# Performance work log

Hardware: AMD Instinct MI355X
Metric: run time of the kernel (lower is better)

The kernel has to match this reference:

```python
import jax, jax.numpy as jnp
from jax import lax
import numpy as np

NUM_HEADS = 8
PATCH = 16
EPS_SUM = 1e-6


def resize_nearest(x, H, W):
    # torch F.interpolate(mode='nearest'): src = floor(dst * in / out)
    ih, iw = x.shape[-2], x.shape[-1]
    ri = (jnp.arange(H) * ih) // H
    ci = (jnp.arange(W) * iw) // W
    return x[:, :, ri][:, :, :, ci]


def single_scale(x, delta, wq, bq, ws, bs):
    # x: [1+K, C, H, W]; delta: [K, 1, H0, W0]
    q, s = x[:1], x[1:]
    K, C, H, W = s.shape
    d = C // NUM_HEADS
    P = PATCH
    Hp, Wp = H // P, W // P
    S = P * P
    delta = resize_nearest(delta, H, W)  # [K,1,H,W]

    qf = jnp.transpose(q, (0, 2, 3, 1))[0] @ wq.T + bq            # [H,W,C]
    qh = qf.reshape(H, W, NUM_HEADS, d).transpose(2, 0, 1, 3)     # [h,H,W,d]
    sf = jnp.transpose(s, (0, 2, 3, 1)) @ ws.T + bs               # [K,H,W,C]
    sh = sf.reshape(K, H, W, NUM_HEADS, d).transpose(0, 3, 1, 2, 4)  # [K,h,H,W,d]

    fg = delta.reshape(K, P, Hp, P, Wp).transpose(0, 1, 3, 2, 4).reshape(K, S, Hp * Wp)
    bg = 1.0 - fg
    fg_sum = jnp.maximum(fg.sum(-1), EPS_SUM)  # [K,S]
    bg_sum = jnp.maximum(bg.sum(-1), EPS_SUM)

    sp = sh.reshape(K, NUM_HEADS, P, Hp, P, Wp, d).transpose(0, 1, 2, 4, 3, 5, 6)
    sp = sp.reshape(K, NUM_HEADS, S, Hp * Wp, d)  # [K,h,S,l,d]

    c_fg = jnp.einsum('ksl,khsld->khsd', fg, sp) / fg_sum[:, None, :, None]
    c_bg = jnp.einsum('ksl,khsld->khsd', bg, sp) / bg_sum[:, None, :, None]
    # concat along prototype dim then flatten as [h, K*2S, d] (K-major, fg-then-bg)
    c_s = jnp.concatenate([c_fg, c_bg], axis=2).transpose(1, 0, 2, 3).reshape(NUM_HEADS, K * 2 * S, d)
    v = jnp.concatenate([jnp.ones((K, S), c_s.dtype), jnp.zeros((K, S), c_s.dtype)], axis=1).reshape(-1)  # [K*2S]

    mask = jnp.concatenate([
        jnp.where(fg_sum < 1.0, -jnp.inf, 0.0),
        jnp.where(bg_sum < 1.0, -jnp.inf, 0.0)], axis=1).reshape(-1)  # [K*2S]

    attn = jnp.einsum('hyxd,hsd->hyxs', qh, c_s) + mask  # [h,H,W,K*2S]
    attn = jax.nn.softmax(attn, axis=-1)
    out = jnp.einsum('hyxs,s->hyx', attn, v)  # [h,H,W]
    return out.mean(0)[None, None]  # [1,1,H,W]


def group_norm(x, gamma, beta, groups=4, eps=1e-5):
    N, C, H, W = x.shape
    xr = x.reshape(N, groups, C // groups, H, W)
    mu = xr.mean((2, 3, 4), keepdims=True)
    var = xr.var((2, 3, 4), keepdims=True)
    xr = (xr - mu) * lax.rsqrt(var + eps)
    return xr.reshape(N, C, H, W) * gamma[None, :, None, None] + beta[None, :, None, None]


def conv2d(x, w, b, pad):
    y = lax.conv_general_dilated(x, w, (1, 1), [(pad, pad), (pad, pad)],
                                 dimension_numbers=('NCHW', 'OIHW', 'NCHW'))
    return y + b[None, :, None, None]


def setup_inputs() -> dict:
    key = jax.random.key(0)
    ks = jax.random.split(key, 24)
    K, C, H, W = 5, 256, 64, 64
    inp = {}
    for i in range(4):
        inp[f'x{i}'] = jax.random.normal(ks[i], (1 + K, C, H, W), jnp.float32)
    inp['delta_onehot_x'] = jax.random.randint(ks[4], (K, 1, 256, 256), 0, 2).astype(jnp.float32)
    inp['wq'] = jax.random.normal(ks[5], (C, C), jnp.float32) * 0.02
    inp['bq'] = jnp.zeros((C,), jnp.float32)
    inp['ws'] = jax.random.normal(ks[6], (C, C), jnp.float32) * 0.02
    inp['bs'] = jnp.zeros((C,), jnp.float32)
    inp['cw1'] = jax.random.normal(ks[7], (16, 4, 5, 5), jnp.float32) * 0.05
    inp['cb1'] = jnp.zeros((16,), jnp.float32)
    inp['g1'] = jnp.ones((16,), jnp.float32)
    inp['be1'] = jnp.zeros((16,), jnp.float32)
    inp['cw2'] = jax.random.normal(ks[8], (64, 16, 5, 5), jnp.float32) * 0.05
    inp['cb2'] = jnp.zeros((64,), jnp.float32)
    inp['g2'] = jnp.ones((64,), jnp.float32)
    inp['be2'] = jnp.zeros((64,), jnp.float32)
    inp['cw3'] = jax.random.normal(ks[9], (128, 64, 3, 3), jnp.float32) * 0.05
    inp['cb3'] = jnp.zeros((128,), jnp.float32)
    inp['g3'] = jnp.ones((128,), jnp.float32)
    inp['be3'] = jnp.zeros((128,), jnp.float32)
    return inp


def reference(x0, x1, x2, x3, delta_onehot_x, wq, bq, ws, bs,
              cw1, cb1, g1, be1, cw2, cb2, g2, be2, cw3, cb3, g3, be3):
    masks = [single_scale(x, delta_onehot_x, wq, bq, ws, bs) for x in (x0, x1, x2, x3)]
    cm = jnp.concatenate(masks, axis=1)  # [1, nlayers=4, H, W]
    # idx=1 conv head: kernels [5,5,3], channels [16,64,128], GroupNorm(4)+ReLU
    h = jax.nn.relu(group_norm(conv2d(cm, cw1, cb1, 2), g1, be1))
    h = jax.nn.relu(group_norm(conv2d(h, cw2, cb2, 2), g2, be2))
    h = jax.nn.relu(group_norm(conv2d(h, cw3, cb3, 1), g3, be3))
    return h
```

## Files before the change

kernel.cpp:

```cpp
#include <hip/hip_runtime.h>
#include <hip/hip_bf16.h>
#include <stdint.h>

#define CCH 256
#define NPIX 4096
#define NH 8
#define M2 2560
#define LOG2E 1.44269504088896f

typedef __attribute__((ext_vector_type(8))) short short8;
typedef __attribute__((ext_vector_type(4))) float f32x4;

__device__ __forceinline__ uint16_t f2bfu(float f) {
    uint32_t u = __builtin_bit_cast(uint32_t, f);
    return (uint16_t)((u + 0x7FFFu + ((u >> 16) & 1u)) >> 16);
}
__device__ __forceinline__ uint32_t pack_bf2(float a, float b) {
    return (uint32_t)f2bfu(a) | ((uint32_t)f2bfu(b) << 16);
}
__device__ __forceinline__ short8 u4_to_s8(uint4 v) {
    return __builtin_bit_cast(short8, v);
}

__device__ __forceinline__ void prep_w_one(const float* __restrict__ w, uint16_t* __restrict__ Wk,
                                           int idx, int Cin, int Cout, int K2) {
    int kk = idx & 31;
    int oc = (idx >> 5) % Cout;
    int ck = idx / (32 * Cout);
    int k = ck * 32 + kk;
    int tap = k / Cin, ic = k % Cin;
    float v = (tap < K2) ? w[((size_t)oc * Cin + ic) * K2 + tap] : 0.0f;
    Wk[idx] = f2bfu(v);
}

__global__ void prep_all(const float* __restrict__ wq, const float* __restrict__ wsm,
                         const float* __restrict__ cw1, const float* __restrict__ cw2,
                         const float* __restrict__ cw3,
                         uint16_t* __restrict__ WB, uint16_t* __restrict__ Wk1,
                         uint16_t* __restrict__ Wk2, uint16_t* __restrict__ Wk3) {
    int idx = blockIdx.x * 256 + threadIdx.x;
    if (idx < 131072) {
        const float* src = (idx < 65536) ? wq : wsm;
        WB[idx] = f2bfu(src[idx & 65535]);
        return;
    }
    idx -= 131072;
    if (idx < 2048)  { prep_w_one(cw1, Wk1, idx, 4, 16, 25);  return; }
    idx -= 2048;
    if (idx < 26624) { prep_w_one(cw2, Wk2, idx, 16, 64, 25); return; }
    idx -= 26624;
    if (idx < 73728) { prep_w_one(cw3, Wk3, idx, 64, 128, 9); return; }
}

__global__ __launch_bounds__(256) void patch_sum(
        const float* __restrict__ x0, const float* __restrict__ x1,
        const float* __restrict__ x2, const float* __restrict__ x3,
        const float* __restrict__ dox, uint16_t* __restrict__ PS,
        float* __restrict__ inv, float* __restrict__ mexpb) {
    int z = blockIdx.z;
    int sc = z / 5, k = z % 5;
    const float* xim = ((sc == 0) ? x0 : (sc == 1) ? x1 : (sc == 2) ? x2 : x3)
                       + (size_t)(k + 1) * CCH * NPIX;
    int p1 = blockIdx.x, chq = blockIdx.y;
    int tid = threadIdx.x;
    int cloc = tid >> 6, col = tid & 63;
    __shared__ float wls[4][64];
    __shared__ uint16_t pst[2][16][72];
    wls[cloc][col] = dox[(size_t)k * 65536 + (size_t)(16 * p1 + 4 * cloc) * 256 + 4 * col];
    __syncthreads();
    float w0 = wls[0][col], w1 = wls[1][col], w2 = wls[2][col], w3 = wls[3][col];
    const float* xbase = xim + p1 * 256 + col;
#pragma unroll 4
    for (int it = 0; it < 16; ++it) {
        int c = chq * 64 + it * 4 + cloc;
        const float* xp = xbase + (size_t)c * NPIX;
        float v0 = xp[0], v1 = xp[64], v2 = xp[128], v3 = xp[192];
        float pf = w0 * v0 + w1 * v1 + w2 * v2 + w3 * v3;
        float pb = (v0 + v1 + v2 + v3) - pf;
        pf += __shfl_xor(pf, 1); pf += __shfl_xor(pf, 2);
        pb += __shfl_xor(pb, 1); pb += __shfl_xor(pb, 2);
        if ((col & 3) == 0) {
            int q = col >> 2, cl = it * 4 + cloc;
            pst[0][q][cl] = f2bfu(pf);
            pst[1][q][cl] = f2bfu(pb);
        }
    }
    if (chq == 0 && tid < 64) {
        float ws = w0 + w1 + w2 + w3;
        ws += __shfl_xor(ws, 1); ws += __shfl_xor(ws, 2);
        if ((col & 3) == 0) {
            int s = p1 * 16 + (col >> 2);
            float fsum = ws, bsum = 16.f - ws;
            int mf = k * 512 + s, mbk = mf + 256;
            mexpb[sc * M2 + mf]  = (fsum < 1.f) ? 0.f : 1.f;
            mexpb[sc * M2 + mbk] = (bsum < 1.f) ? 0.f : 1.f;
            inv[(size_t)(z * 2 + 0) * 256 + s] = 1.f / fmaxf(fsum, 1e-6f);
            inv[(size_t)(z * 2 + 1) * 256 + s] = 1.f / fmaxf(bsum, 1e-6f);
        }
    }
    __syncthreads();
    int fb = tid >> 7, rem = tid & 127;
    int q = rem >> 3, chunk = rem & 7;
    uint4 v = *(const uint4*)&pst[fb][q][chunk * 8];
    int s = p1 * 16 + q;
    *(uint4*)&PS[((size_t)(z * 2 + fb) * 256 + s) * CCH + chq * 64 + chunk * 8] = v;
}

__global__ __launch_bounds__(256) void cent_gemm(
        const uint16_t* __restrict__ PS, const uint16_t* __restrict__ WB,
        const float* __restrict__ bs, const float* __restrict__ inv,
        uint16_t* __restrict__ Csbf) {
    int tid = threadIdx.x, lane = tid & 63, wid = tid >> 6;
    int lp = lane & 15, g = lane >> 4;
    int rowb = blockIdx.x * 128 + wid * 32;
    int cob = blockIdx.y * 64;
    const uint16_t* wsb = WB + 65536;
    f32x4 acc[2][4] = {};
#pragma unroll
    for (int ks = 0; ks < 8; ++ks) {
        int k0 = ks * 32;
        uint4 a0 = *(const uint4*)(PS + (size_t)(rowb + lp) * CCH + k0 + g * 8);
        uint4 a1 = *(const uint4*)(PS + (size_t)(rowb + 16 + lp) * CCH + k0 + g * 8);
        short8 af[2] = {u4_to_s8(a0), u4_to_s8(a1)};
        short8 b[4];
#pragma unroll
        for (int t = 0; t < 4; ++t) {
            uint4 bw = *(const uint4*)(wsb + (size_t)(cob + t * 16 + lp) * 256 + k0 + g * 8);
            b[t] = u4_to_s8(bw);
        }
#pragma unroll
        for (int m = 0; m < 2; ++m)
#pragma unroll
            for (int t = 0; t < 4; ++t)
                acc[m][t] = __builtin_amdgcn_mfma_f32_16x16x32_bf16(af[m], b[t], acc[m][t], 0, 0, 0);
    }
#pragma unroll
    for (int m = 0; m < 2; ++m)
#pragma unroll
        for (int t = 0; t < 4; ++t) {
            int co = cob + t * 16 + lp;
            int h = co >> 5, d = co & 31;
            float bv = bs[co];
#pragma unroll
            for (int r = 0; r < 4; ++r) {
                int row = rowb + m * 16 + g * 4 + r;
                int zz = row >> 9, fb = (row >> 8) & 1, s = row & 255;
                int scc = zz / 5, kk = zz % 5;
                int slot = kk * 512 + fb * 256 + s;
                float val = acc[m][t][r] * inv[row] + bv;
                Csbf[(((size_t)scc * NH + h) * M2 + slot) * 32 + d] = f2bfu(val);
            }
        }
}

__global__ __launch_bounds__(512) void q_gemm(
        const float* __restrict__ x0, const float* __restrict__ x1,
        const float* __restrict__ x2, const float* __restrict__ x3,
        const uint16_t* __restrict__ WB, const float* __restrict__ bq,
        uint16_t* __restrict__ Qbf) {
    int sc = blockIdx.y;
    const float* xim = (sc == 0) ? x0 : (sc == 1) ? x1 : (sc == 2) ? x2 : x3;
    int p0 = blockIdx.x * 64;
    int tid = threadIdx.x, lane = tid & 63, wid = tid >> 6;
    int lp = lane & 15, g = lane >> 4;
    int wm = wid >> 1, wn = wid & 1;
    __shared__ uint32_t Al[16][68];
    f32x4 acc[8] = {};
#pragma unroll
    for (int ks = 0; ks < 8; ++ks) {
        int k0 = ks * 32;
        __syncthreads();
        if (tid < 256) {
            int rp = tid >> 4, f4i = tid & 15;
            float4 v0 = *(const float4*)(xim + (size_t)(k0 + 2 * rp) * NPIX + p0 + f4i * 4);
            float4 v1 = *(const float4*)(xim + (size_t)(k0 + 2 * rp + 1) * NPIX + p0 + f4i * 4);
            *(uint4*)&Al[rp][f4i * 4] = make_uint4(
                pack_bf2(v0.x, v1.x), pack_bf2(v0.y, v1.y),
                pack_bf2(v0.z, v1.z), pack_bf2(v0.w, v1.w));
        }
        __syncthreads();
        short8 b[8];
#pragma unroll
        for (int tn = 0; tn < 8; ++tn) {
            uint4 bw = *(const uint4*)(WB + (size_t)(wn * 128 + tn * 16 + lp) * 256 + k0 + g * 8);
            b[tn] = u4_to_s8(bw);
        }
        int px = wm * 16 + lp;
        uint4 av = make_uint4(Al[4 * g + 0][px], Al[4 * g + 1][px],
                              Al[4 * g + 2][px], Al[4 * g + 3][px]);
        short8 af = u4_to_s8(av);
#pragma unroll
        for (int tn = 0; tn < 8; ++tn)
            acc[tn] = __builtin_amdgcn_mfma_f32_16x16x32_bf16(af, b[tn], acc[tn], 0, 0, 0);
    }
#pragma unroll
    for (int tn = 0; tn < 8; ++tn) {
        int co = wn * 128 + tn * 16 + lp;
        float bv = bq[co];
#pragma unroll
        for (int r = 0; r < 4; ++r) {
            int row = p0 + wm * 16 + g * 4 + r;
            Qbf[((size_t)(sc * NPIX + row)) * CCH + co] = f2bfu((acc[tn][r] + bv) * LOG2E);
        }
    }
}

__global__ __launch_bounds__(256) void attn_v6(
        const uint16_t* __restrict__ Qbf, const uint16_t* __restrict__ Csbf,
        const float* __restrict__ mexpb, float* __restrict__ sfbuf) {
    int head = blockIdx.y;
    int sc = blockIdx.z >> 2, split = blockIdx.z & 3;
    int tid = threadIdx.x;
    int lane = tid & 63, wid = tid >> 6;
    int lp = lane & 15, g = lane >> 4;
    int p0w = blockIdx.x * 256 + wid * 64;

    const uint16_t* Qs = Qbf + (size_t)sc * NPIX * CCH;
    const uint16_t* csb = Csbf + ((size_t)sc * NH + head) * M2 * 32;
    const float* mb = mexpb + sc * M2;

    short8 aq[4];
#pragma unroll
    for (int m = 0; m < 4; m++) {
        uint4 qv = *(const uint4*)(Qs + (size_t)(p0w + m * 16 + lp) * CCH + head * 32 + g * 8);
        aq[m] = u4_to_s8(qv);
    }

    const f32x4 zero4 = {0.f, 0.f, 0.f, 0.f};
    float sfg[4][4] = {}, sbg[4][4] = {};
    int cbeg = split * 640;
    for (int c0loc = 0; c0loc < 640; c0loc += 64) {
        int c0 = cbeg + c0loc;
        bool fg = ((c0 & 511) < 256);
        short8 bf[4];
        float mexp[4];
#pragma unroll
        for (int t = 0; t < 4; t++) {
            int row = c0 + t * 16 + lp;
            bf[t] = u4_to_s8(*(const uint4*)(csb + (size_t)row * 32 + g * 8));
            mexp[t] = mb[row];
        }
        if (fg) {
#pragma unroll
            for (int m = 0; m < 4; m++)
#pragma unroll
                for (int t = 0; t < 4; t++) {
                    f32x4 c = __builtin_amdgcn_mfma_f32_16x16x32_bf16(aq[m], bf[t], zero4, 0, 0, 0);
#pragma unroll
                    for (int r = 0; r < 4; r++)
                        sfg[m][r] = fmaf(__builtin_amdgcn_exp2f(c[r]), mexp[t], sfg[m][r]);
                }
        } else {
#pragma unroll
            for (int m = 0; m < 4; m++)
#pragma unroll
                for (int t = 0; t < 4; t++) {
                    f32x4 c = __builtin_amdgcn_mfma_f32_16x16x32_bf16(aq[m], bf[t], zero4, 0, 0, 0);
#pragma unroll
                    for (int r = 0; r < 4; r++)
                        sbg[m][r] = fmaf(__builtin_amdgcn_exp2f(c[r]), mexp[t], sbg[m][r]);
                }
        }
    }
#pragma unroll
    for (int m = 0; m < 4; m++)
#pragma unroll
        for (int r = 0; r < 4; r++) {
#pragma unroll
            for (int msk = 1; msk < 16; msk <<= 1) {
                sfg[m][r] += __shfl_xor(sfg[m][r], msk);
                sbg[m][r] += __shfl_xor(sbg[m][r], msk);
            }
        }
    if (lp == 0) {
        float* sf = sfbuf + (size_t)((sc * 4 + split) * 2) * NH * NPIX;
        float* so = sf + (size_t)head * NPIX;
        float* fo = sf + (size_t)(NH + head) * NPIX;
#pragma unroll
        for (int m = 0; m < 4; m++)
#pragma unroll
            for (int r = 0; r < 4; r++) {
                int px = p0w + m * 16 + g * 4 + r;
                so[px] = sfg[m][r] + sbg[m][r];
                fo[px] = sfg[m][r];
            }
    }
}

__global__ void mean_heads3(const float* __restrict__ sfbuf, float* __restrict__ cm) {
    int idx = blockIdx.x * 256 + threadIdx.x;
    int sc = idx >> 12, p = idx & 4095;
    const float* b = sfbuf + (size_t)sc * 4 * 2 * NH * NPIX;
    float acc = 0.f;
#pragma unroll
    for (int h = 0; h < NH; h++) {
        float sv = 0.f, fv = 0.f;
#pragma unroll
        for (int sp = 0; sp < 4; sp++) {
            sv += b[((size_t)(sp * 2) * NH + h) * NPIX + p];
            fv += b[((size_t)(sp * 2 + 1) * NH + h) * NPIX + p];
        }
        acc += fv / sv;
    }
    cm[idx] = 0.125f * acc;
}

template<int CIN, int COUT, int KSZ, int NPIN, int NPOUT, bool GNIN>
__global__ __launch_bounds__(256) void conv_mfma(
        const float* __restrict__ in, const uint16_t* __restrict__ Wk,
        const float* __restrict__ bias,
        const float* __restrict__ gin, const float* __restrict__ bein,
        const float2* __restrict__ pin,
        float* __restrict__ out, float2* __restrict__ pout) {
    constexpr int PAD = KSZ / 2;
    constexpr int NTAP = KSZ * KSZ;
    constexpr int K = CIN * NTAP;
    constexpr int CK = (K + 31) / 32;
    constexpr int PXP = 64 + 2 * PAD;
    constexpr int ICB = (CIN >= 8) ? CIN / 8 : 1;
    __shared__ uint16_t Xs[KSZ * PXP * CIN];
    __shared__ float gaL[CIN], beL[CIN];
    __shared__ float gmu[4], grs[4];
    int tid = threadIdx.x;
    int lane = tid & 63, wv = tid >> 6;
    int lp = lane & 15, g = lane >> 4;
    int y = blockIdx.x;
    int oc0 = blockIdx.y * 64;

    if (GNIN) {
        float s = 0.f, s2 = 0.f;
        for (int i = lane; i < NPIN; i += 64) {
            float2 p = pin[wv * NPIN + i];
            s += p.x; s2 += p.y;
        }
#pragma unroll
        for (int m = 32; m; m >>= 1) { s += __shfl_xor(s, m); s2 += __shfl_xor(s2, m); }
        if (lane == 0) {
            float n = (float)((CIN / 4) * NPIX);
            float mu = s / n;
            gmu[wv] = mu;
            grs[wv] = rsqrtf(s2 / n - mu * mu + 1e-5f);
        }
        __syncthreads();
        if (tid < CIN) {
            int gg = tid / (CIN / 4);
            float ga = gin[tid] * grs[gg];
            gaL[tid] = ga;
            beL[tid] = bein[tid] - gmu[gg] * ga;
        }
        __syncthreads();
    }

    if (CIN >= 8) {
        for (int idx = tid; idx < KSZ * ICB * PXP; idx += 256) {
            int pxp = idx % PXP; int rem = idx / PXP;
            int icb = rem % ICB; int r = rem / ICB;
            int gy = y + r - PAD, gx = pxp - PAD;
            bool ok = ((unsigned)gy < 64u) && ((unsigned)gx < 64u);
            const float* ip = in + (size_t)(icb * 8) * NPIX + gy * 64 + gx;
            uint32_t wb[4];
#pragma unroll
            for (int j = 0; j < 4; j++) {
                int c0c = icb * 8 + 2 * j, c1c = c0c + 1;
                float v0 = ok ? ip[(size_t)(2 * j) * NPIX] : 0.f;
                float v1 = ok ? ip[(size_t)(2 * j + 1) * NPIX] : 0.f;
                if (GNIN) {
                    v0 = fmaf(v0, gaL[c0c], beL[c0c]); v0 = v0 > 0.f ? v0 : 0.f;
                    v1 = fmaf(v1, gaL[c1c], beL[c1c]); v1 = v1 > 0.f ? v1 : 0.f;
                    if (!ok) { v0 = 0.f; v1 = 0.f; }
                }
                wb[j] = pack_bf2(v0, v1);
            }
            *(uint4*)&Xs[(size_t)idx * 8] = make_uint4(wb[0], wb[1], wb[2], wb[3]);
        }
    } else {
        for (int idx = tid; idx < KSZ * PXP; idx += 256) {
            int pxp = idx % PXP; int r = idx / PXP;
            int gy = y + r - PAD, gx = pxp - PAD;
            bool ok = ((unsigned)gy < 64u) && ((unsigned)gx < 64u);
            const float* ip = in + (size_t)gy * 64 + gx;
            float v0 = ok ? ip[0] : 0.f, v1 = ok ? ip[NPIX] : 0.f;
            float v2 = ok ? ip[2 * NPIX] : 0.f, v3 = ok ? ip[3 * NPIX] : 0.f;
            *(uint2*)&Xs[(size_t)idx * 4] = make_uint2(pack_bf2(v0, v1), pack_bf2(v2, v3));
        }
    }
    __syncthreads();

    int tmb, tme, tn;
    if (COUT >= 64) { tn = wv; tmb = 0; tme = 4; }
    else            { tn = 0;  tmb = wv; tme = wv + 1; }
    int oc = oc0 + tn * 16 + lp;
    f32x4 acc[4] = {};

#pragma unroll
    for (int ck = 0; ck < CK; ck++) {
        const uint16_t* wp = Wk + ((size_t)ck * COUT + oc) * 32 + g * 8;
        uint4 bw = *(const uint4*)wp;
        short8 bfr = u4_to_s8(bw);
        if (CIN >= 8) {
            int gk = ck * 4 + g;
            int tap = gk / ICB; if (tap > NTAP - 1) tap = NTAP - 1;
            int icb = gk % ICB;
            int r = tap / KSZ, dx = tap % KSZ;
            int base = (r * ICB + icb) * PXP * 8;
            for (int tm = tmb; tm < tme; tm++) {
                int pxp = tm * 16 + lp + dx;
                uint4 av = *(const uint4*)&Xs[base + pxp * 8];
                short8 afr = u4_to_s8(av);
                acc[tm] = __builtin_amdgcn_mfma_f32_16x16x32_bf16(afr, bfr, acc[tm], 0, 0, 0);
            }
        } else {
            int gk = ck * 4 + g;
            int t0 = 2 * gk;     if (t0 > NTAP - 1) t0 = NTAP - 1;
            int t1 = 2 * gk + 1; if (t1 > NTAP - 1) t1 = NTAP - 1;
            int r0 = t0 / KSZ, dx0 = t0 % KSZ;
            int r1 = t1 / KSZ, dx1 = t1 % KSZ;
            for (int tm = tmb; tm < tme; tm++) {
                uint2 a0 = *(const uint2*)&Xs[((size_t)(r0 * PXP + tm * 16 + lp + dx0)) * 4];
                uint2 a1 = *(const uint2*)&Xs[((size_t)(r1 * PXP + tm * 16 + lp + dx1)) * 4];
                uint4 av = make_uint4(a0.x, a0.y, a1.x, a1.y);
                short8 afr = u4_to_s8(av);
                acc[tm] = __builtin_amdgcn_mfma_f32_16x16x32_bf16(afr, bfr, acc[tm], 0, 0, 0);
            }
        }
    }
    float bv = bias[oc];
    float ps = 0.f, ps2 = 0.f;
    for (int tm = tmb; tm < tme; tm++)
#pragma unroll
        for (int r = 0; r < 4; r++) {
            int px = tm * 16 + g * 4 + r;
            float val = acc[tm][r] + bv;
            out[(size_t)oc * NPIX + y * 64 + px] = val;
            ps += val;
            ps2 = fmaf(val, val, ps2);
        }
    if (COUT >= 64) {
#pragma unroll
        for (int m = 32; m; m >>= 1) { ps += __shfl_xor(ps, m); ps2 += __shfl_xor(ps2, m); }
        if (lane == 0) {
            if (COUT == 64) {
                pout[wv * NPOUT + y] = make_float2(ps, ps2);
            } else {
                int grp = blockIdx.y * 2 + (wv >> 1);
                pout[grp * NPOUT + y * 2 + (wv & 1)] = make_float2(ps, ps2);
            }
        }
    } else {
#pragma unroll
        for (int m : {1, 2, 16, 32}) { ps += __shfl_xor(ps, m); ps2 += __shfl_xor(ps2, m); }
        int q = (lane >> 2) & 3;
        if (lane == q * 4)
            pout[q * NPOUT + y * 4 + wv] = make_float2(ps, ps2);
    }
}

__global__ __launch_bounds__(256) void gn_apply_relu(const float* __restrict__ in, const float2* __restrict__ part,
                                                     const float* __restrict__ gamma, const float* __restrict__ beta,
                                                     int Cg, int npart, float* __restrict__ out) {
    int idx4 = blockIdx.x * 256 + threadIdx.x;
    int c = idx4 >> 10;
    int g = c / Cg;
    float s = 0.0f, s2 = 0.0f;
    for (int b = 0; b < npart; b++) {
        float2 p = part[g * npart + b];
        s += p.x; s2 += p.y;
    }
    float n = (float)(Cg * NPIX);
    float mu = s / n;
    float rstd = rsqrtf(s2 / n - mu * mu + 1e-5f);
    float ga = gamma[c] * rstd;
    float be = beta[c] - mu * ga;
    float4 v = ((const float4*)in)[idx4];
    float4 o;
    o.x = fmaf(v.x, ga, be); o.x = o.x > 0.f ? o.x : 0.f;
    o.y = fmaf(v.y, ga, be); o.y = o.y > 0.f ? o.y : 0.f;
    o.z = fmaf(v.z, ga, be); o.z = o.z > 0.f ? o.z : 0.f;
    o.w = fmaf(v.w, ga, be); o.w = o.w > 0.f ? o.w : 0.f;
    ((float4*)out)[idx4] = o;
}

extern "C" void kernel_launch(void* const* d_in, const int* in_sizes, int n_in,
                              void* d_out, int out_size, void* d_ws, size_t ws_size,
                              hipStream_t stream) {
    const float* x0 = (const float*)d_in[0];
    const float* x1 = (const float*)d_in[1];
    const float* x2 = (const float*)d_in[2];
    const float* x3 = (const float*)d_in[3];
    const float* dox = (const float*)d_in[4];
    const float* wq  = (const float*)d_in[5];
    const float* bq  = (const float*)d_in[6];
    const float* wsm = (const float*)d_in[7];
    const float* bs  = (const float*)d_in[8];
    const float* cw1 = (const float*)d_in[9];
    const float* cb1 = (const float*)d_in[10];
    const float* g1  = (const float*)d_in[11];
    const float* be1 = (const float*)d_in[12];
    const float* cw2 = (const float*)d_in[13];
    const float* cb2 = (const float*)d_in[14];
    const float* g2  = (const float*)d_in[15];
    const float* be2 = (const float*)d_in[16];
    const float* cw3 = (const float*)d_in[17];
    const float* cb3 = (const float*)d_in[18];
    const float* g3  = (const float*)d_in[19];
    const float* be3 = (const float*)d_in[20];

    uint16_t* Qbf  = (uint16_t*)d_ws;
    uint16_t* Csbf = Qbf + (size_t)4194304;
    uint16_t* PS   = Csbf + (size_t)2621440;
    uint16_t* WB   = PS + (size_t)2621440;
    uint16_t* Wk1  = WB + 131072;
    uint16_t* Wk2  = Wk1 + 2048;
    uint16_t* Wk3  = Wk2 + 26624;
    float* fbase  = (float*)(Wk3 + 73728);
    float* mexpb  = fbase;
    float* inv    = mexpb + 10240;
    float* sfbuf  = inv + 10240;
    float* cm     = sfbuf + 1048576;
    float* h1     = cm + 16384;
    float* h2     = h1 + 65536;
    float* h3     = h2 + 262144;
    float2* part1 = (float2*)(h3 + 524288);
    float2* part2 = part1 + 4 * 256;
    float2* part3 = part2 + 4 * 64;

    prep_all<<<(233472 + 255) / 256, 256, 0, stream>>>(wq, wsm, cw1, cw2, cw3, WB, Wk1, Wk2, Wk3);

    patch_sum<<<dim3(16, 4, 20), 256, 0, stream>>>(x0, x1, x2, x3, dox, PS, inv, mexpb);
    q_gemm<<<dim3(64, 4), 512, 0, stream>>>(x0, x1, x2, x3, WB, bq, Qbf);
    cent_gemm<<<dim3(80, 4), 256, 0, stream>>>(PS, WB, bs, inv, Csbf);
    attn_v6<<<dim3(16, NH, 16), 256, 0, stream>>>(Qbf, Csbf, mexpb, sfbuf);
    mean_heads3<<<64, 256, 0, stream>>>(sfbuf, cm);

    conv_mfma<4, 16, 5, 1, 256, false><<<dim3(64, 1), 256, 0, stream>>>(
        cm, Wk1, cb1, nullptr, nullptr, nullptr, h1, part1);
    conv_mfma<16, 64, 5, 256, 64, true><<<dim3(64, 1), 256, 0, stream>>>(
        h1, Wk2, cb2, g1, be1, part1, h2, part2);
    conv_mfma<64, 128, 3, 64, 128, true><<<dim3(64, 2), 256, 0, stream>>>(
        h2, Wk3, cb3, g2, be2, part2, h3, part3);
    gn_apply_relu<<<(128 * 1024) / 256, 256, 0, stream>>>(h3, part3, g3, be3, 32, 128, (float*)d_out);
}
```

Measured before the change: 144.6 us.

## Fuse weight prep, patch sums and Q GEMM into one front-end launch

Merges the weight-conversion kernel, the patch-sum kernel and the query projection GEMM into a single 512-thread kernel whose block index selects the role. The Q GEMM now reads fp32 wq directly and converts to bf16 in registers, which removes its dependency on the prepped weights so all three parts can run concurrently. Patch-sum blocks are widened to handle two channel quarters each. This removes two launch boundaries and lets independent work overlap, at the cost of redundant per-block weight conversion and heterogeneous blocks sharing one register and LDS budget.

```diff
diff --git a/kernel.cpp b/kernel.cpp
--- a/kernel.cpp
+++ b/kernel.cpp
@@ -20,6 +20,11 @@
 }
 __device__ __forceinline__ short8 u4_to_s8(uint4 v) {
     return __builtin_bit_cast(short8, v);
+}
+__device__ __forceinline__ short8 mk8(uint32_t a, uint32_t b, uint32_t c, uint32_t d) {
+    union { uint32_t u[4]; short8 s; } t;
+    t.u[0] = a; t.u[1] = b; t.u[2] = c; t.u[3] = d;
+    return t.s;
 }
 
 __device__ __forceinline__ void prep_w_one(const float* __restrict__ w, uint16_t* __restrict__ Wk,
@@ -33,77 +38,137 @@
     Wk[idx] = f2bfu(v);
 }
 
-__global__ void prep_all(const float* __restrict__ wq, const float* __restrict__ wsm,
-                         const float* __restrict__ cw1, const float* __restrict__ cw2,
-                         const float* __restrict__ cw3,
-                         uint16_t* __restrict__ WB, uint16_t* __restrict__ Wk1,
-                         uint16_t* __restrict__ Wk2, uint16_t* __restrict__ Wk3) {
-    int idx = blockIdx.x * 256 + threadIdx.x;
-    if (idx < 131072) {
-        const float* src = (idx < 65536) ? wq : wsm;
-        WB[idx] = f2bfu(src[idx & 65535]);
-        return;
-    }
-    idx -= 131072;
-    if (idx < 2048)  { prep_w_one(cw1, Wk1, idx, 4, 16, 25);  return; }
-    idx -= 2048;
-    if (idx < 26624) { prep_w_one(cw2, Wk2, idx, 16, 64, 25); return; }
-    idx -= 26624;
-    if (idx < 73728) { prep_w_one(cw3, Wk3, idx, 64, 128, 9); return; }
-}
-
-__global__ __launch_bounds__(256) void patch_sum(
+__global__ __launch_bounds__(512) void fused_front(
         const float* __restrict__ x0, const float* __restrict__ x1,
         const float* __restrict__ x2, const float* __restrict__ x3,
-        const float* __restrict__ dox, uint16_t* __restrict__ PS,
-        float* __restrict__ inv, float* __restrict__ mexpb) {
-    int z = blockIdx.z;
-    int sc = z / 5, k = z % 5;
-    const float* xim = ((sc == 0) ? x0 : (sc == 1) ? x1 : (sc == 2) ? x2 : x3)
-                       + (size_t)(k + 1) * CCH * NPIX;
-    int p1 = blockIdx.x, chq = blockIdx.y;
+        const float* __restrict__ dox,
+        const float* __restrict__ wq, const float* __restrict__ bq,
+        const float* __restrict__ wsm,
+        const float* __restrict__ cw1, const float* __restrict__ cw2, const float* __restrict__ cw3,
+        uint16_t* __restrict__ PS, float* __restrict__ inv, float* __restrict__ mexpb,
+        uint16_t* __restrict__ Qbf,
+        uint16_t* __restrict__ WB, uint16_t* __restrict__ Wk1,
+        uint16_t* __restrict__ Wk2, uint16_t* __restrict__ Wk3) {
+    int b = blockIdx.x;
     int tid = threadIdx.x;
-    int cloc = tid >> 6, col = tid & 63;
     __shared__ float wls[4][64];
-    __shared__ uint16_t pst[2][16][72];
-    wls[cloc][col] = dox[(size_t)k * 65536 + (size_t)(16 * p1 + 4 * cloc) * 256 + 4 * col];
-    __syncthreads();
-    float w0 = wls[0][col], w1 = wls[1][col], w2 = wls[2][col], w3 = wls[3][col];
-    const float* xbase = xim + p1 * 256 + col;
+    __shared__ uint16_t pst[2][2][16][72];
+    __shared__ uint32_t Al[16][68];
+
+    if (b < 640) {
+        int z = b >> 5, rem_b = b & 31;
+        int p1 = rem_b & 15, chqh = rem_b >> 4;
+        int hg = tid >> 8, t2 = tid & 255;
+        int chq = chqh * 2 + hg;
+        int sc = z / 5, k = z % 5;
+        const float* xim = ((sc == 0) ? x0 : (sc == 1) ? x1 : (sc == 2) ? x2 : x3)
+                           + (size_t)(k + 1) * CCH * NPIX;
+        int cloc = t2 >> 6, col = t2 & 63;
+        if (tid < 256)
+            wls[cloc][col] = dox[(size_t)k * 65536 + (size_t)(16 * p1 + 4 * cloc) * 256 + 4 * col];
+        __syncthreads();
+        float w0 = wls[0][col], w1 = wls[1][col], w2 = wls[2][col], w3 = wls[3][col];
+        const float* xbase = xim + p1 * 256 + col;
 #pragma unroll 4
-    for (int it = 0; it < 16; ++it) {
-        int c = chq * 64 + it * 4 + cloc;
-        const float* xp = xbase + (size_t)c * NPIX;
-        float v0 = xp[0], v1 = xp[64], v2 = xp[128], v3 = xp[192];
-        float pf = w0 * v0 + w1 * v1 + w2 * v2 + w3 * v3;
-        float pb = (v0 + v1 + v2 + v3) - pf;
-        pf += __shfl_xor(pf, 1); pf += __shfl_xor(pf, 2);
-        pb += __shfl_xor(pb, 1); pb += __shfl_xor(pb, 2);
-        if ((col & 3) == 0) {
-            int q = col >> 2, cl = it * 4 + cloc;
-            pst[0][q][cl] = f2bfu(pf);
-            pst[1][q][cl] = f2bfu(pb);
-        }
-    }
-    if (chq == 0 && tid < 64) {
-        float ws = w0 + w1 + w2 + w3;
-        ws += __shfl_xor(ws, 1); ws += __shfl_xor(ws, 2);
-        if ((col & 3) == 0) {
-            int s = p1 * 16 + (col >> 2);
-            float fsum = ws, bsum = 16.f - ws;
-            int mf = k * 512 + s, mbk = mf + 256;
-            mexpb[sc * M2 + mf]  = (fsum < 1.f) ? 0.f : 1.f;
-            mexpb[sc * M2 + mbk] = (bsum < 1.f) ? 0.f : 1.f;
-            inv[(size_t)(z * 2 + 0) * 256 + s] = 1.f / fmaxf(fsum, 1e-6f);
-            inv[(size_t)(z * 2 + 1) * 256 + s] = 1.f / fmaxf(bsum, 1e-6f);
-        }
-    }
-    __syncthreads();
-    int fb = tid >> 7, rem = tid & 127;
-    int q = rem >> 3, chunk = rem & 7;
-    uint4 v = *(const uint4*)&pst[fb][q][chunk * 8];
-    int s = p1 * 16 + q;
-    *(uint4*)&PS[((size_t)(z * 2 + fb) * 256 + s) * CCH + chq * 64 + chunk * 8] = v;
+        for (int it = 0; it < 16; ++it) {
+            int c = chq * 64 + it * 4 + cloc;
+            const float* xp = xbase + (size_t)c * NPIX;
+            float v0 = xp[0], v1 = xp[64], v2 = xp[128], v3 = xp[192];
+            float pf = w0 * v0 + w1 * v1 + w2 * v2 + w3 * v3;
+            float pb = (v0 + v1 + v2 + v3) - pf;
+            pf += __shfl_xor(pf, 1); pf += __shfl_xor(pf, 2);
+            pb += __shfl_xor(pb, 1); pb += __shfl_xor(pb, 2);
+            if ((col & 3) == 0) {
+                int q = col >> 2, cl = it * 4 + cloc;
+                pst[hg][0][q][cl] = f2bfu(pf);
+                pst[hg][1][q][cl] = f2bfu(pb);
+            }
+        }
+        if (chq == 0 && t2 < 64 && tid < 64) {
+            float ws = w0 + w1 + w2 + w3;
+            ws += __shfl_xor(ws, 1); ws += __shfl_xor(ws, 2);
+            if ((col & 3) == 0) {
+                int s = p1 * 16 + (col >> 2);
+                float fsum = ws, bsum = 16.f - ws;
+                int mf = k * 512 + s, mbk = mf + 256;
+                mexpb[sc * M2 + mf]  = (fsum < 1.f) ? 0.f : 1.f;
+                mexpb[sc * M2 + mbk] = (bsum < 1.f) ? 0.f : 1.f;
+                inv[(size_t)(z * 2 + 0) * 256 + s] = 1.f / fmaxf(fsum, 1e-6f);
+                inv[(size_t)(z * 2 + 1) * 256 + s] = 1.f / fmaxf(bsum, 1e-6f);
+            }
+        }
+        __syncthreads();
+        int fb = t2 >> 7, rem = t2 & 127;
+        int q = rem >> 3, chunk = rem & 7;
+        uint4 v = *(const uint4*)&pst[hg][fb][q][chunk * 8];
+        int s = p1 * 16 + q;
+        *(uint4*)&PS[((size_t)(z * 2 + fb) * 256 + s) * CCH + chq * 64 + chunk * 8] = v;
+    } else if (b < 896) {
+        int bb = b - 640;
+        int sc = bb >> 6;
+        int p0 = (bb & 63) * 64;
+        const float* xim = (sc == 0) ? x0 : (sc == 1) ? x1 : (sc == 2) ? x2 : x3;
+        int lane = tid & 63, wid = tid >> 6;
+        int lp = lane & 15, g = lane >> 4;
+        int wm = wid >> 1, wn = wid & 1;
+        f32x4 acc[8] = {};
+#pragma unroll
+        for (int ks = 0; ks < 8; ++ks) {
+            int k0 = ks * 32;
+            __syncthreads();
+            if (tid < 256) {
+                int rp = tid >> 4, f4i = tid & 15;
+                float4 v0 = *(const float4*)(xim + (size_t)(k0 + 2 * rp) * NPIX + p0 + f4i * 4);
+                float4 v1 = *(const float4*)(xim + (size_t)(k0 + 2 * rp + 1) * NPIX + p0 + f4i * 4);
+                *(uint4*)&Al[rp][f4i * 4] = make_uint4(
+                    pack_bf2(v0.x, v1.x), pack_bf2(v0.y, v1.y),
+                    pack_bf2(v0.z, v1.z), pack_bf2(v0.w, v1.w));
+            }
+            __syncthreads();
+            short8 bfr[8];
+#pragma unroll
+            for (int tn = 0; tn < 8; ++tn) {
+                const float* wr = wq + (size_t)(wn * 128 + tn * 16 + lp) * 256 + k0 + g * 8;
+                float4 f0 = *(const float4*)wr;
+                float4 f1 = *(const float4*)(wr + 4);
+                bfr[tn] = mk8(pack_bf2(f0.x, f0.y), pack_bf2(f0.z, f0.w),
+                              pack_bf2(f1.x, f1.y), pack_bf2(f1.z, f1.w));
+            }
+            int px = wm * 16 + lp;
+            uint4 av = make_uint4(Al[4 * g + 0][px], Al[4 * g + 1][px],
+                                  Al[4 * g + 2][px], Al[4 * g + 3][px]);
+            short8 af = u4_to_s8(av);
+#pragma unroll
+            for (int tn = 0; tn < 8; ++tn)
+                acc[tn] = __builtin_amdgcn_mfma_f32_16x16x32_bf16(af, bfr[tn], acc[tn], 0, 0, 0);
+        }
+#pragma unroll
+        for (int tn = 0; tn < 8; ++tn) {
+            int co = wn * 128 + tn * 16 + lp;
+            float bv = bq[co];
+#pragma unroll
+            for (int r = 0; r < 4; ++r) {
+                int row = p0 + wm * 16 + g * 4 + r;
+                Qbf[((size_t)(sc * NPIX + row)) * CCH + co] = f2bfu((acc[tn][r] + bv) * LOG2E);
+            }
+        }
+    } else {
+        int idx0 = (b - 896) * 512 + tid;
+        for (int i = idx0; i < 233472; i += 65536) {
+            int idx = i;
+            if (idx < 131072) {
+                const float* src = (idx < 65536) ? wq : wsm;
+                WB[idx] = f2bfu(src[idx & 65535]);
+                continue;
+            }
+            idx -= 131072;
+            if (idx < 2048)  { prep_w_one(cw1, Wk1, idx, 4, 16, 25);  continue; }
+            idx -= 2048;
+            if (idx < 26624) { prep_w_one(cw2, Wk2, idx, 16, 64, 25); continue; }
+            idx -= 26624;
+            if (idx < 73728) { prep_w_one(cw3, Wk3, idx, 64, 128, 9); continue; }
+        }
+    }
 }
 
 __global__ __launch_bounds__(256) void cent_gemm(
@@ -151,58 +216,6 @@
                 Csbf[(((size_t)scc * NH + h) * M2 + slot) * 32 + d] = f2bfu(val);
             }
         }
-}
-
-__global__ __launch_bounds__(512) void q_gemm(
-        const float* __restrict__ x0, const float* __restrict__ x1,
-        const float* __restrict__ x2, const float* __restrict__ x3,
-        const uint16_t* __restrict__ WB, const float* __restrict__ bq,
-        uint16_t* __restrict__ Qbf) {
-    int sc = blockIdx.y;
-    const float* xim = (sc == 0) ? x0 : (sc == 1) ? x1 : (sc == 2) ? x2 : x3;
-    int p0 = blockIdx.x * 64;
-    int tid = threadIdx.x, lane = tid & 63, wid = tid >> 6;
-    int lp = lane & 15, g = lane >> 4;
-    int wm = wid >> 1, wn = wid & 1;
-    __shared__ uint32_t Al[16][68];
-    f32x4 acc[8] = {};
-#pragma unroll
-    for (int ks = 0; ks < 8; ++ks) {
-        int k0 = ks * 32;
-        __syncthreads();
-        if (tid < 256) {
-            int rp = tid >> 4, f4i = tid & 15;
-            float4 v0 = *(const float4*)(xim + (size_t)(k0 + 2 * rp) * NPIX + p0 + f4i * 4);
-            float4 v1 = *(const float4*)(xim + (size_t)(k0 + 2 * rp + 1) * NPIX + p0 + f4i * 4);
-            *(uint4*)&Al[rp][f4i * 4] = make_uint4(
-                pack_bf2(v0.x, v1.x), pack_bf2(v0.y, v1.y),
-                pack_bf2(v0.z, v1.z), pack_bf2(v0.w, v1.w));
-        }
-        __syncthreads();
-        short8 b[8];
-#pragma unroll
-        for (int tn = 0; tn < 8; ++tn) {
-            uint4 bw = *(const uint4*)(WB + (size_t)(wn * 128 + tn * 16 + lp) * 256 + k0 + g * 8);
-            b[tn] = u4_to_s8(bw);
-        }
-        int px = wm * 16 + lp;
-        uint4 av = make_uint4(Al[4 * g + 0][px], Al[4 * g + 1][px],
-                              Al[4 * g + 2][px], Al[4 * g + 3][px]);
-        short8 af = u4_to_s8(av);
-#pragma unroll
-        for (int tn = 0; tn < 8; ++tn)
-            acc[tn] = __builtin_amdgcn_mfma_f32_16x16x32_bf16(af, b[tn], acc[tn], 0, 0, 0);
-    }
-#pragma unroll
-    for (int tn = 0; tn < 8; ++tn) {
-        int co = wn * 128 + tn * 16 + lp;
-        float bv = bq[co];
-#pragma unroll
-        for (int r = 0; r < 4; ++r) {
-            int row = p0 + wm * 16 + g * 4 + r;
-            Qbf[((size_t)(sc * NPIX + row)) * CCH + co] = f2bfu((acc[tn][r] + bv) * LOG2E);
-        }
-    }
 }
 
 __global__ __launch_bounds__(256) void attn_v6(
@@ -524,10 +537,10 @@
     float2* part2 = part1 + 4 * 256;
     float2* part3 = part2 + 4 * 64;
 
-    prep_all<<<(233472 + 255) / 256, 256, 0, stream>>>(wq, wsm, cw1, cw2, cw3, WB, Wk1, Wk2, Wk3);
-
-    patch_sum<<<dim3(16, 4, 20), 256, 0, stream>>>(x0, x1, x2, x3, dox, PS, inv, mexpb);
-    q_gemm<<<dim3(64, 4), 512, 0, stream>>>(x0, x1, x2, x3, WB, bq, Qbf);
+    fused_front<<<1024, 512, 0, stream>>>(x0, x1, x2, x3, dox, wq, bq, wsm,
+                                          cw1, cw2, cw3,
+                                          PS, inv, mexpb, Qbf, WB, Wk1, Wk2, Wk3);
+
     cent_gemm<<<dim3(80, 4), 256, 0, stream>>>(PS, WB, bs, inv, Csbf);
     attn_v6<<<dim3(16, NH, 16), 256, 0, stream>>>(Qbf, Csbf, mexpb, sfbuf);
     mean_heads3<<<64, 256, 0, stream>>>(sfbuf, cm);
```

Result: slower. 163.6 us (+13.2%).
